# Kernel tuning notes

Hardware: AMD Instinct MI355X
Metric: run time of the kernel (lower is better)

Reference implementation:

```python
import jax, jax.numpy as jnp
import numpy as np

H_DIM = 128
EMB = 16
MODES = 6
TRAJ = MODES * 2  # 12
PRED_LEN = 30
B = 65536
NEG_SLOPE = 0.01  # F.leaky_relu default


def setup_inputs() -> dict:
    key = jax.random.key(0)
    ks = jax.random.split(key, 16)
    s = lambda k, shape, fan_in: jax.random.uniform(k, shape, jnp.float32, -1.0, 1.0) / np.sqrt(fan_in)
    return {
        "last_obs": jax.random.normal(ks[0], (B, 2), jnp.float32),
        "last_obs_rel": jax.random.normal(ks[1], (B, 2), jnp.float32),
        "h0": jax.random.normal(ks[2], (1, B, H_DIM), jnp.float32),
        "c0": jax.random.normal(ks[3], (1, B, H_DIM), jnp.float32),
        # nn.LSTM(EMB, H_DIM, 1): weight_ih (4H, EMB), weight_hh (4H, H), biases (4H,)
        "W_ih": s(ks[4], (4 * H_DIM, EMB), H_DIM),
        "W_hh": s(ks[5], (4 * H_DIM, H_DIM), H_DIM),
        "b_ih": s(ks[6], (4 * H_DIM,), H_DIM),
        "b_hh": s(ks[7], (4 * H_DIM,), H_DIM),
        # spatial_embedding: Linear(TRAJ, EMB)
        "W_emb": s(ks[8], (EMB, TRAJ), TRAJ),
        "b_emb": s(ks[9], (EMB,), TRAJ),
        # hidden2pos: Linear(H_DIM, TRAJ)
        "W_pos": s(ks[10], (TRAJ, H_DIM), H_DIM),
        "b_pos": s(ks[11], (TRAJ,), H_DIM),
        # confidences: Linear(H_DIM, MODES)
        "W_conf": s(ks[12], (MODES, H_DIM), H_DIM),
        "b_conf": s(ks[13], (MODES,), H_DIM),
    }


def _lstm_cell(x, h, c, W_ih, W_hh, b):
    # x: (B, EMB), h/c: (B, H). PyTorch gate order: i, f, g, o
    gates = x @ W_ih.T + h @ W_hh.T + b  # (B, 4H)
    i, f, g, o = jnp.split(gates, 4, axis=-1)
    c_new = jax.nn.sigmoid(f) * c + jax.nn.sigmoid(i) * jnp.tanh(g)
    h_new = jax.nn.sigmoid(o) * jnp.tanh(c_new)
    return h_new, c_new


def reference(last_obs, last_obs_rel, h0, c0, W_ih, W_hh, b_ih, b_hh,
              W_emb, b_emb, W_pos, b_pos, W_conf, b_conf):
    b_gate = b_ih + b_hh
    batch = last_obs_rel.shape[0]
    # repeat_interleave last_obs_rel over modes -> (B, 12)
    rel0 = jnp.repeat(last_obs_rel[:, None, :], MODES, axis=1).reshape(batch, TRAJ)
    dec_in = jax.nn.leaky_relu(rel0 @ W_emb.T + b_emb, NEG_SLOPE)  # (B, EMB); eval mode => no dropout

    def step(carry, _):
        h, c, x = carry
        h, c = _lstm_cell(x, h, c, W_ih, W_hh, b_gate)
        rel_pos = h @ W_pos.T + b_pos                                # (B, TRAJ)
        x_next = jax.nn.leaky_relu(rel_pos @ W_emb.T + b_emb, NEG_SLOPE)
        return (h, c, x_next), rel_pos

    (_, _, _), rels = jax.lax.scan(step, (h0[0], c0[0], dec_in), None, length=PRED_LEN)
    # rels: (PRED_LEN, B, TRAJ) -> (B, MODES, PRED_LEN, 2)
    pred = rels.reshape(PRED_LEN, batch, MODES, 2).transpose(1, 2, 0, 3)
    # conf uses the ORIGINAL (un-updated) state_tuple_h, as in the source
    conf = jax.nn.softmax(h0[0] @ W_conf.T + b_conf, axis=1)         # (B, MODES)
    return pred, conf
```

## Files before the change

kernel.cpp:

```cpp
#include <hip/hip_runtime.h>

typedef _Float16 f16;
typedef f16 f16x2 __attribute__((ext_vector_type(2)));
typedef f16 f16x4 __attribute__((ext_vector_type(4)));
typedef f16 f16x8 __attribute__((ext_vector_type(8)));
typedef float f32x4 __attribute__((ext_vector_type(4)));
typedef int i32x4 __attribute__((ext_vector_type(4)));
typedef __fp16 fp16x2_raw __attribute__((ext_vector_type(2)));

#define MT 64
#define NSTEP 30
#define LOG2E 1.4426950408889634f

__device__ __forceinline__ float rcp_f(float x) { return __builtin_amdgcn_rcpf(x); }
__device__ __forceinline__ float exp2_f(float x) {
#if __has_builtin(__builtin_amdgcn_exp2f)
    return __builtin_amdgcn_exp2f(x);
#else
    return __builtin_exp2f(x);
#endif
}
__device__ __forceinline__ int pk2i(float a, float b) {
    fp16x2_raw t = __builtin_amdgcn_cvt_pkrtz(a, b);
    return __builtin_bit_cast(int, t);
}
__device__ __forceinline__ f16x4 pk4(float a, float b, float c, float d) {
    int lo = pk2i(a, b), hi = pk2i(c, d);
    int2 t = {lo, hi};
    return __builtin_bit_cast(f16x4, t);
}

__global__ __launch_bounds__(512) void mdlstm_kernel(
    const float* __restrict__ lor,
    const float* __restrict__ h0,
    const float* __restrict__ c0,
    const float* __restrict__ W_ih,
    const float* __restrict__ W_hh,
    const float* __restrict__ b_ih, const float* __restrict__ b_hh,
    const float* __restrict__ W_emb,
    const float* __restrict__ b_emb,
    const float* __restrict__ W_pos,
    const float* __restrict__ b_pos,
    const float* __restrict__ W_conf,
    const float* __restrict__ b_conf,
    float* __restrict__ out, int batch)
{
    __shared__ f16 h_lds[2 * MT * 128];
    __shared__ f16 wpos_lds[4 * 64 * 8];
    __shared__ f16 weu_lds[4 * 64 * 8];
    __shared__ f16 x0_lds[MT * 16];
    __shared__ float bu_lds[16];
    __shared__ float bp_lds[16];

    char* hb  = (char*)h_lds;
    char* wpb = (char*)wpos_lds;
    char* wub = (char*)weu_lds;
    char* x0b = (char*)x0_lds;
    char* bub = (char*)bu_lds;
    char* bpb = (char*)bp_lds;

    const int tid = threadIdx.x;
    const int wv  = tid >> 6;
    const int ln  = tid & 63;
    const int g   = ln >> 4;
    const int q   = ln & 15;
    const int b0  = blockIdx.x * MT;
    if (b0 >= batch) return;

    const float gsc[4] = {-LOG2E, -LOG2E, 2.f * LOG2E, -LOG2E};

    f16x8 whh[4][4];
    #pragma unroll
    for (int g4 = 0; g4 < 4; ++g4) {
        const int col = g4 * 128 + wv * 16 + q;
        #pragma unroll
        for (int kf = 0; kf < 4; ++kf) {
            const float* p = W_hh + col * 128 + kf * 32 + g * 8;
            f16x8 v;
            #pragma unroll
            for (int j = 0; j < 8; ++j) v[j] = (f16)(p[j] * gsc[g4]);
            whh[g4][kf] = v;
        }
    }
    f16x8 wih[4];
    #pragma unroll
    for (int g4 = 0; g4 < 4; ++g4) {
        const int col = g4 * 128 + wv * 16 + q;
        f16x8 v = {};
        if (g < 2) {
            const float* p = W_ih + col * 16 + g * 8;
            #pragma unroll
            for (int j = 0; j < 8; ++j) v[j] = (f16)(p[j] * gsc[g4]);
        } else if (g == 2) {
            v[0] = (f16)((b_ih[col] + b_hh[col]) * gsc[g4]);
        }
        wih[g4] = v;
    }

    if (tid < 16) {
        float s = b_emb[tid];
        #pragma unroll
        for (int p = 0; p < 12; ++p) s += W_emb[tid * 12 + p] * b_pos[p];
        bu_lds[tid] = s;
        bp_lds[tid] = (tid < 12) ? b_pos[tid] : 0.f;
    }

    if (wv == 0) {
        #pragma unroll
        for (int kf = 0; kf < 4; ++kf) {
            f16x8 v = {};
            if (q < 12) {
                const float* p = W_pos + q * 128 + kf * 32 + g * 8;
                #pragma unroll
                for (int j = 0; j < 8; ++j) v[j] = (f16)p[j];
            }
            *(f16x8*)(wpb + kf * 1024 + ln * 16) = v;
        }
        float we_q[12];
        #pragma unroll
        for (int p = 0; p < 12; ++p) we_q[p] = W_emb[q * 12 + p];
        #pragma unroll
        for (int kf = 0; kf < 4; ++kf) {
            f16x8 v;
            #pragma unroll
            for (int j = 0; j < 8; ++j) {
                const int k = kf * 32 + g * 8 + j;
                float s = 0.f;
                #pragma unroll
                for (int p = 0; p < 12; ++p) s += we_q[p] * W_pos[p * 128 + k];
                v[j] = (f16)s;
            }
            *(f16x8*)(wub + kf * 1024 + ln * 16) = v;
        }
    }

    f32x4 c_st[4];
    #pragma unroll
    for (int mt = 0; mt < 4; ++mt)
        c_st[mt] = *(const f32x4*)(c0 + (size_t)(b0 + 16 * mt + q) * 128 + 16 * wv + 4 * g);

    const int swz = (q & 7) << 5;
    int rdbase[4];
    #pragma unroll
    for (int kf = 0; kf < 4; ++kf) rdbase[kf] = q * 256 + ((kf * 64 + g * 16) ^ swz);
    const int wrb = q * 256 + ((wv * 32 + g * 8) ^ swz);
    const int src0 = ((g & 1) << 5) | q;
    const int src1 = src0 + 16;

    int pz = 0;

    float* outp = out + (size_t)(b0 + 16 * wv + q) * 360 + 2 * g * 60;

    {
        const int row = tid >> 3, seg = tid & 7;
        const float* p = h0 + (size_t)(b0 + row) * 128 + seg * 16;
        const int rswz = (row & 7) << 5;
        #pragma unroll
        for (int hh2 = 0; hh2 < 2; ++hh2) {
            f16x8 v;
            #pragma unroll
            for (int j = 0; j < 8; ++j) v[j] = (f16)p[hh2 * 8 + j];
            const int off = row * 256 + (((seg * 4 + 2 * hh2) * 8) ^ rswz);
            *(f16x8*)(hb + off) = v;
        }
    }

    if (wv < 4) {
        f16x8 wemb = {};
        #pragma unroll
        for (int j = 0; j < 8; ++j) {
            const int k = g * 8 + j;
            if (k < 12) wemb[j] = (f16)W_emb[q * 12 + k];
        }
        const float2 xy = *(const float2*)(lor + (size_t)(b0 + 16 * wv + q) * 2);
        f16x8 rf = {};
        if (g < 2) {
            #pragma unroll
            for (int j = 0; j < 8; ++j) {
                const int k = g * 8 + j;
                if (k < 12) rf[j] = (f16)((k & 1) ? xy.y : xy.x);
            }
        }
        f32x4 u0;
        #pragma unroll
        for (int r = 0; r < 4; ++r) u0[r] = b_emb[4 * g + r];
        u0 = __builtin_amdgcn_mfma_f32_16x16x32_f16(wemb, rf, u0, 0, 0, 0);
        *(f16x4*)(x0b + (16 * wv + q) * 32 + g * 8) =
            pk4(fmaxf(u0[0], .01f * u0[0]), fmaxf(u0[1], .01f * u0[1]),
                fmaxf(u0[2], .01f * u0[2]), fmaxf(u0[3], .01f * u0[3]));
    }

    {
        const int e  = tid >> 3;
        const int p8 = tid & 7;
        const float* hp = h0 + (size_t)(b0 + e) * 128 + p8 * 16;
        float pc[6];
        #pragma unroll
        for (int md = 0; md < 6; ++md) {
            const float* wc = W_conf + md * 128 + p8 * 16;
            float s = 0.f;
            #pragma unroll
            for (int i = 0; i < 16; ++i) s += hp[i] * wc[i];
            pc[md] = s;
        }
        #pragma unroll
        for (int md = 0; md < 6; ++md) {
            pc[md] += __shfl_down(pc[md], 4, 8);
            pc[md] += __shfl_down(pc[md], 2, 8);
            pc[md] += __shfl_down(pc[md], 1, 8);
        }
        if (p8 == 0) {
            float mx = -1e30f;
            #pragma unroll
            for (int md = 0; md < 6; ++md) { pc[md] += b_conf[md]; mx = fmaxf(mx, pc[md]); }
            float s = 0.f;
            #pragma unroll
            for (int md = 0; md < 6; ++md) { pc[md] = __expf(pc[md] - mx); s += pc[md]; }
            const float rs = rcp_f(s);
            float* cp = out + (size_t)batch * 360 + (size_t)(b0 + e) * 6;
            #pragma unroll
            for (int md = 0; md < 6; ++md) cp[md] = pc[md] * rs;
        }
    }

    __syncthreads();

#define STEP(BR, BW, T_, FIRST) do {                                            \
    asm volatile("" : "+v"(pz));                                                \
    const int wuoff = ln * 16 + pz;              \
    const int boff  = g * 16 + pz;               \
    _Pragma("unroll")                                                           \
    for (int mt = 0; mt < 4; ++mt) {                                            \
        f32x4 a0 = {0,0,0,0}, a1 = {0,0,0,0}, a2 = {0,0,0,0}, a3 = {0,0,0,0};   \
        f32x4 uacc;                                                             \
        if (FIRST) uacc = a0;                                                   \
        else       uacc = *(const f32x4*)(bub + boff);                          \
        _Pragma("unroll")                                                       \
        for (int kf = 0; kf < 4; ++kf) {                                        \
            f16x8 hf = *(const f16x8*)(hb + (BR) + mt * 4096 + rdbase[kf]);     \
            a0 = __builtin_amdgcn_mfma_f32_16x16x32_f16(whh[0][kf], hf, a0, 0, 0, 0); \
            a1 = __builtin_amdgcn_mfma_f32_16x16x32_f16(whh[1][kf], hf, a1, 0, 0, 0); \
            a2 = __builtin_amdgcn_mfma_f32_16x16x32_f16(whh[2][kf], hf, a2, 0, 0, 0); \
            a3 = __builtin_amdgcn_mfma_f32_16x16x32_f16(whh[3][kf], hf, a3, 0, 0, 0); \
            if (!(FIRST)) {                                                     \
                f16x8 wu = *(const f16x8*)(wub + wuoff + kf * 1024);            \
                uacc = __builtin_amdgcn_mfma_f32_16x16x32_f16(wu, hf, uacc, 0, 0, 0); \
            }                                                                   \
        }                                                                       \
        f16x8 xf;                                                               \
        if (FIRST) {                                                            \
            i32x4 xw = {0, 0, 0, 0};                                            \
            if (g < 2)       xw = *(const i32x4*)(x0b + (mt * 16 + q) * 32 + g * 16); \
            else if (g == 2) xw[0] = 0x3C00;                                    \
            xf = __builtin_bit_cast(f16x8, xw);                                 \
        } else {                                                                \
            const int d0i = pk2i(fmaxf(uacc[0], .01f * uacc[0]), fmaxf(uacc[1], .01f * uacc[1])); \
            const int d1i = pk2i(fmaxf(uacc[2], .01f * uacc[2]), fmaxf(uacc[3], .01f * uacc[3])); \
            i32x4 xw;                                                           \
            xw[0] = __shfl(d0i, src0, 64);                                      \
            xw[1] = __shfl(d1i, src0, 64);                                      \
            xw[2] = __shfl(d0i, src1, 64);                                      \
            xw[3] = __shfl(d1i, src1, 64);                                      \
            if (g == 2)      { xw[0] = 0x3C00; xw[1] = 0; xw[2] = 0; xw[3] = 0; } \
            else if (g == 3) { xw[0] = 0; xw[1] = 0; xw[2] = 0; xw[3] = 0; }    \
            xf = __builtin_bit_cast(f16x8, xw);                                 \
        }                                                                       \
        a0 = __builtin_amdgcn_mfma_f32_16x16x32_f16(wih[0], xf, a0, 0, 0, 0);   \
        a1 = __builtin_amdgcn_mfma_f32_16x16x32_f16(wih[1], xf, a1, 0, 0, 0);   \
        a2 = __builtin_amdgcn_mfma_f32_16x16x32_f16(wih[2], xf, a2, 0, 0, 0);   \
        a3 = __builtin_amdgcn_mfma_f32_16x16x32_f16(wih[3], xf, a3, 0, 0, 0);   \
        f32x4 hv;                                                               \
        _Pragma("unroll")                                                       \
        for (int r = 0; r < 4; ++r) {                                           \
            const float ei = exp2_f(a0[r]);                                     \
            const float ef = exp2_f(a1[r]);                                     \
            const float eg = exp2_f(a2[r]);                                     \
            const float eo = exp2_f(a3[r]);                                     \
            const float pi = 1.f + ei, pf = 1.f + ef, pg = 1.f + eg;            \
            const float t1 = pi * pg;                                           \
            const float R1 = rcp_f(t1 * pf);                                    \
            const float sf = t1 * R1;                                           \
            const float itg = (eg - 1.f) * (pf * R1);                           \
            const float cv = sf * c_st[mt][r] + itg;                            \
            c_st[mt][r] = cv;                                                   \
            const float ec = exp2_f(fminf(cv, 30.f) * (2.f * LOG2E));           \
            const float R2 = rcp_f((1.f + eo) * (1.f + ec));                    \
            hv[r] = (ec - 1.f) * R2;                                            \
        }                                                                       \
        *(f16x4*)(hb + (BW) + mt * 4096 + wrb) = pk4(hv[0], hv[1], hv[2], hv[3]); \
    }                                                                           \
    if (!(FIRST) && wv < 4) {     \
        f32x4 racc = *(const f32x4*)(bpb + boff);                               \
        _Pragma("unroll")                                                       \
        for (int kf = 0; kf < 4; ++kf) {                                        \
            f16x8 wp = *(const f16x8*)(wpb + wuoff + kf * 1024);                \
            f16x8 hf = *(const f16x8*)(hb + (BR) + wv * 4096 + rdbase[kf]);     \
            racc = __builtin_amdgcn_mfma_f32_16x16x32_f16(wp, hf, racc, 0, 0, 0); \
        }                                                                       \
        if (g < 3) {                                                            \
            float2 s0 = {racc[0], racc[1]};                                     \
            float2 s1 = {racc[2], racc[3]};                                     \
            float* pp = outp + 2 * ((T_) - 1);                                  \
            *(float2*)pp = s0;                                                  \
            *(float2*)(pp + 60) = s1;                                           \
        }                                                                       \
    }                                                                           \
    __syncthreads();                                                            \
} while (0)

    STEP(0, 16384, 0, true);
    #pragma unroll 1
    for (int tt = 1; tt < NSTEP - 1; tt += 2) {
        STEP(16384, 0, tt, false);
        STEP(0, 16384, tt + 1, false);
    }
    STEP(16384, 0, NSTEP - 1, false);

    if (wv < 4) {
        asm volatile("" : "+v"(pz));
        const int wuoff = ln * 16 + pz;
        const int boff  = g * 16 + pz;
        f32x4 racc = *(const f32x4*)(bpb + boff);
        #pragma unroll
        for (int kf = 0; kf < 4; ++kf) {
            f16x8 wp = *(const f16x8*)(wpb + wuoff + kf * 1024);
            f16x8 hf = *(const f16x8*)(hb + wv * 4096 + rdbase[kf]);
            racc = __builtin_amdgcn_mfma_f32_16x16x32_f16(wp, hf, racc, 0, 0, 0);
        }
        if (g < 3) {
            float2 s0 = {racc[0], racc[1]};
            float2 s1 = {racc[2], racc[3]};
            float* pp = outp + 2 * (NSTEP - 1);
            *(float2*)pp = s0;
            *(float2*)(pp + 60) = s1;
        }
    }
#undef STEP
}

extern "C" void kernel_launch(void* const* d_in, const int* in_sizes, int n_in,
                              void* d_out, int out_size, void* d_ws, size_t ws_size,
                              hipStream_t stream) {
    const float* last_obs_rel = (const float*)d_in[1];
    const float* h0     = (const float*)d_in[2];
    const float* c0     = (const float*)d_in[3];
    const float* W_ih   = (const float*)d_in[4];
    const float* W_hh   = (const float*)d_in[5];
    const float* b_ih   = (const float*)d_in[6];
    const float* b_hh   = (const float*)d_in[7];
    const float* W_emb  = (const float*)d_in[8];
    const float* b_emb  = (const float*)d_in[9];
    const float* W_pos  = (const float*)d_in[10];
    const float* b_pos  = (const float*)d_in[11];
    const float* W_conf = (const float*)d_in[12];
    const float* b_conf = (const float*)d_in[13];
    float* out = (float*)d_out;

    const int batch = in_sizes[1] / 2;
    const int grid  = (batch + MT - 1) / MT;
    mdlstm_kernel<<<grid, 512, 0, stream>>>(last_obs_rel, h0, c0, W_ih, W_hh,
                                            b_ih, b_hh, W_emb, b_emb, W_pos,
                                            b_pos, W_conf, b_conf, out, batch);
}
```

Before: 524.5 us.

## Split embedding update and output projection across wave groups after each step

The next-step input embedding (W_emb·W_pos fused matmul plus leaky-ReLU) is moved out of the per-wave gate loop. It is now computed once per step by waves 4-7 from the freshly written h and staged through LDS, while waves 0-3 compute the position output in parallel. Before, every wave redundantly recomputed the embedding MFMA for all four row tiles and exchanged results with shuffles. The trade is a second __syncthreads per step and an LDS round trip in exchange for fewer MFMAs on the critical path.

```diff
diff --git a/kernel.cpp b/kernel.cpp
--- a/kernel.cpp
+++ b/kernel.cpp
@@ -48,14 +48,14 @@
     __shared__ f16 h_lds[2 * MT * 128];
     __shared__ f16 wpos_lds[4 * 64 * 8];
     __shared__ f16 weu_lds[4 * 64 * 8];
-    __shared__ f16 x0_lds[MT * 16];
+    __shared__ f16 x_lds[MT * 16];
     __shared__ float bu_lds[16];
     __shared__ float bp_lds[16];
 
     char* hb  = (char*)h_lds;
     char* wpb = (char*)wpos_lds;
     char* wub = (char*)weu_lds;
-    char* x0b = (char*)x0_lds;
+    char* xb  = (char*)x_lds;
     char* bub = (char*)bu_lds;
     char* bpb = (char*)bp_lds;
 
@@ -144,8 +144,7 @@
     #pragma unroll
     for (int kf = 0; kf < 4; ++kf) rdbase[kf] = q * 256 + ((kf * 64 + g * 16) ^ swz);
     const int wrb = q * 256 + ((wv * 32 + g * 8) ^ swz);
-    const int src0 = ((g & 1) << 5) | q;
-    const int src1 = src0 + 16;
+    const int xrd = q * 32 + g * 16;
 
     int pz = 0;
 
@@ -185,7 +184,7 @@
         #pragma unroll
         for (int r = 0; r < 4; ++r) u0[r] = b_emb[4 * g + r];
         u0 = __builtin_amdgcn_mfma_f32_16x16x32_f16(wemb, rf, u0, 0, 0, 0);
-        *(f16x4*)(x0b + (16 * wv + q) * 32 + g * 8) =
+        *(f16x4*)(xb + (16 * wv + q) * 32 + g * 8) =
             pk4(fmaxf(u0[0], .01f * u0[0]), fmaxf(u0[1], .01f * u0[1]),
                 fmaxf(u0[2], .01f * u0[2]), fmaxf(u0[3], .01f * u0[3]));
     }
@@ -225,16 +224,14 @@
 
     __syncthreads();
 
-#define STEP(BR, BW, T_, FIRST) do {                                            \
+#define STEP(BR, BW, T_, LAST) do {                                             \
     asm volatile("" : "+v"(pz));                                                \
     const int wuoff = ln * 16 + pz;              \
     const int boff  = g * 16 + pz;               \
+     \
     _Pragma("unroll")                                                           \
     for (int mt = 0; mt < 4; ++mt) {                                            \
         f32x4 a0 = {0,0,0,0}, a1 = {0,0,0,0}, a2 = {0,0,0,0}, a3 = {0,0,0,0};   \
-        f32x4 uacc;                                                             \
-        if (FIRST) uacc = a0;                                                   \
-        else       uacc = *(const f32x4*)(bub + boff);                          \
         _Pragma("unroll")                                                       \
         for (int kf = 0; kf < 4; ++kf) {                                        \
             f16x8 hf = *(const f16x8*)(hb + (BR) + mt * 4096 + rdbase[kf]);     \
@@ -242,33 +239,17 @@
             a1 = __builtin_amdgcn_mfma_f32_16x16x32_f16(whh[1][kf], hf, a1, 0, 0, 0); \
             a2 = __builtin_amdgcn_mfma_f32_16x16x32_f16(whh[2][kf], hf, a2, 0, 0, 0); \
             a3 = __builtin_amdgcn_mfma_f32_16x16x32_f16(whh[3][kf], hf, a3, 0, 0, 0); \
-            if (!(FIRST)) {                                                     \
-                f16x8 wu = *(const f16x8*)(wub + wuoff + kf * 1024);            \
-                uacc = __builtin_amdgcn_mfma_f32_16x16x32_f16(wu, hf, uacc, 0, 0, 0); \
-            }                                                                   \
-        }                                                                       \
-        f16x8 xf;                                                               \
-        if (FIRST) {                                                            \
+        }                                                                       \
+        {                                                                       \
             i32x4 xw = {0, 0, 0, 0};                                            \
-            if (g < 2)       xw = *(const i32x4*)(x0b + (mt * 16 + q) * 32 + g * 16); \
+            if (g < 2)       xw = *(const i32x4*)(xb + mt * 512 + xrd);         \
             else if (g == 2) xw[0] = 0x3C00;                                    \
-            xf = __builtin_bit_cast(f16x8, xw);                                 \
-        } else {                                                                \
-            const int d0i = pk2i(fmaxf(uacc[0], .01f * uacc[0]), fmaxf(uacc[1], .01f * uacc[1])); \
-            const int d1i = pk2i(fmaxf(uacc[2], .01f * uacc[2]), fmaxf(uacc[3], .01f * uacc[3])); \
-            i32x4 xw;                                                           \
-            xw[0] = __shfl(d0i, src0, 64);                                      \
-            xw[1] = __shfl(d1i, src0, 64);                                      \
-            xw[2] = __shfl(d0i, src1, 64);                                      \
-            xw[3] = __shfl(d1i, src1, 64);                                      \
-            if (g == 2)      { xw[0] = 0x3C00; xw[1] = 0; xw[2] = 0; xw[3] = 0; } \
-            else if (g == 3) { xw[0] = 0; xw[1] = 0; xw[2] = 0; xw[3] = 0; }    \
-            xf = __builtin_bit_cast(f16x8, xw);                                 \
-        }                                                                       \
-        a0 = __builtin_amdgcn_mfma_f32_16x16x32_f16(wih[0], xf, a0, 0, 0, 0);   \
-        a1 = __builtin_amdgcn_mfma_f32_16x16x32_f16(wih[1], xf, a1, 0, 0, 0);   \
-        a2 = __builtin_amdgcn_mfma_f32_16x16x32_f16(wih[2], xf, a2, 0, 0, 0);   \
-        a3 = __builtin_amdgcn_mfma_f32_16x16x32_f16(wih[3], xf, a3, 0, 0, 0);   \
+            const f16x8 xf = __builtin_bit_cast(f16x8, xw);                     \
+            a0 = __builtin_amdgcn_mfma_f32_16x16x32_f16(wih[0], xf, a0, 0, 0, 0); \
+            a1 = __builtin_amdgcn_mfma_f32_16x16x32_f16(wih[1], xf, a1, 0, 0, 0); \
+            a2 = __builtin_amdgcn_mfma_f32_16x16x32_f16(wih[2], xf, a2, 0, 0, 0); \
+            a3 = __builtin_amdgcn_mfma_f32_16x16x32_f16(wih[3], xf, a3, 0, 0, 0); \
+        }                                                                       \
         f32x4 hv;                                                               \
         _Pragma("unroll")                                                       \
         for (int r = 0; r < 4; ++r) {                                           \
@@ -289,51 +270,43 @@
         }                                                                       \
         *(f16x4*)(hb + (BW) + mt * 4096 + wrb) = pk4(hv[0], hv[1], hv[2], hv[3]); \
     }                                                                           \
-    if (!(FIRST) && wv < 4) {     \
+    __syncthreads();                                           \
+     \
+    if (wv < 4) {                                                               \
         f32x4 racc = *(const f32x4*)(bpb + boff);                               \
         _Pragma("unroll")                                                       \
         for (int kf = 0; kf < 4; ++kf) {                                        \
             f16x8 wp = *(const f16x8*)(wpb + wuoff + kf * 1024);                \
-            f16x8 hf = *(const f16x8*)(hb + (BR) + wv * 4096 + rdbase[kf]);     \
+            f16x8 hf = *(const f16x8*)(hb + (BW) + wv * 4096 + rdbase[kf]);     \
             racc = __builtin_amdgcn_mfma_f32_16x16x32_f16(wp, hf, racc, 0, 0, 0); \
         }                                                                       \
         if (g < 3) {                                                            \
             float2 s0 = {racc[0], racc[1]};                                     \
             float2 s1 = {racc[2], racc[3]};                                     \
-            float* pp = outp + 2 * ((T_) - 1);                                  \
+            float* pp = outp + 2 * (T_);                                        \
             *(float2*)pp = s0;                                                  \
             *(float2*)(pp + 60) = s1;                                           \
         }                                                                       \
+    } else if (!(LAST)) {                                                       \
+        const int mt = wv - 4;                                                  \
+        f32x4 uacc = *(const f32x4*)(bub + boff);                               \
+        _Pragma("unroll")                                                       \
+        for (int kf = 0; kf < 4; ++kf) {                                        \
+            f16x8 wu = *(const f16x8*)(wub + wuoff + kf * 1024);                \
+            f16x8 hf = *(const f16x8*)(hb + (BW) + mt * 4096 + rdbase[kf]);     \
+            uacc = __builtin_amdgcn_mfma_f32_16x16x32_f16(wu, hf, uacc, 0, 0, 0); \
+        }                                                                       \
+        *(f16x4*)(xb + (16 * mt + q) * 32 + g * 8) =                            \
+            pk4(fmaxf(uacc[0], .01f * uacc[0]), fmaxf(uacc[1], .01f * uacc[1]), \
+                fmaxf(uacc[2], .01f * uacc[2]), fmaxf(uacc[3], .01f * uacc[3])); \
     }                                                                           \
-    __syncthreads();                                                            \
+    __syncthreads();                 \
 } while (0)
 
-    STEP(0, 16384, 0, true);
     #pragma unroll 1
-    for (int tt = 1; tt < NSTEP - 1; tt += 2) {
-        STEP(16384, 0, tt, false);
-        STEP(0, 16384, tt + 1, false);
-    }
-    STEP(16384, 0, NSTEP - 1, false);
-
-    if (wv < 4) {
-        asm volatile("" : "+v"(pz));
-        const int wuoff = ln * 16 + pz;
-        const int boff  = g * 16 + pz;
-        f32x4 racc = *(const f32x4*)(bpb + boff);
-        #pragma unroll
-        for (int kf = 0; kf < 4; ++kf) {
-            f16x8 wp = *(const f16x8*)(wpb + wuoff + kf * 1024);
-            f16x8 hf = *(const f16x8*)(hb + wv * 4096 + rdbase[kf]);
-            racc = __builtin_amdgcn_mfma_f32_16x16x32_f16(wp, hf, racc, 0, 0, 0);
-        }
-        if (g < 3) {
-            float2 s0 = {racc[0], racc[1]};
-            float2 s1 = {racc[2], racc[3]};
-            float* pp = outp + 2 * (NSTEP - 1);
-            *(float2*)pp = s0;
-            *(float2*)(pp + 60) = s1;
-        }
+    for (int tt = 0; tt < NSTEP; tt += 2) {
+        STEP(0, 16384, tt, false);
+        STEP(16384, 0, tt + 1, (tt + 1 == NSTEP - 1));
     }
 #undef STEP
 }
```

Result: faster. 478.0 us (-8.9%).
